# Kernel tuning notes

Hardware: AMD Instinct MI355X
Metric: run time of the kernel (lower is better)

The kernel has to match this reference:

```python
import jax, jax.numpy as jnp
import numpy as np


def _conv1x1(x, W, b):
    # x: [b,c,h,w], W: [out,in], b: [out]
    return jnp.einsum('oi,bihw->bohw', W, x) + b[None, :, None, None]


def setup_inputs() -> dict:
    key = jax.random.key(0)
    ks = jax.random.split(key, 8)
    B, C, H, W = 4, 256, 64, 64
    s = 1.0 / np.sqrt(C)
    return {
        'x1': jax.random.normal(ks[0], (B, C, H, W), jnp.float32),
        'x2': jax.random.normal(ks[1], (B, C, H, W), jnp.float32),
        'Wq': jax.random.normal(ks[2], (C, C), jnp.float32) * s,
        'bq': jax.random.normal(ks[3], (C,), jnp.float32) * 0.01,
        'Wk': jax.random.normal(ks[4], (C, C), jnp.float32) * s,
        'bk': jax.random.normal(ks[5], (C,), jnp.float32) * 0.01,
        'Wv': jax.random.normal(ks[6], (C, C), jnp.float32) * s,
        'bv': jax.random.normal(ks[7], (C,), jnp.float32) * 0.01,
    }


def reference(x1, x2, Wq, bq, Wk, bk, Wv, bv):
    b, c, h, w = x1.shape
    n = h * w
    q = _conv1x1(x1, Wq, bq).reshape(b, c, n)   # [b,c,n]
    k = _conv1x1(x2, Wk, bk).reshape(b, c, n)   # [b,c,n]
    v = _conv1x1(x2, Wv, bv).reshape(b, c, n)   # [b,c,n]
    # scores[b,i,j] = sum_c q[b,c,i] * k[b,c,j]; softmax over j (last dim)
    scores = jnp.einsum('bci,bcj->bij', q, k)
    attn = jax.nn.softmax(scores, axis=-1)      # [b,n,n]
    # out[b,c,i] = sum_j v[b,c,j] * attn[b,i,j]  (v @ attn^T)
    out = jnp.einsum('bcj,bij->bci', v, attn)
    return out.reshape(b, c, h, w)
```

## Files before the change

### kernel.cpp

```cpp
#include <hip/hip_runtime.h>

#define BATCH 4
#define CDIM 256
#define NDIM 4096
#define SPLITS 4
#define KSPLIT (NDIM / SPLITS)
#define JT 32
#define NTILES (KSPLIT / JT)

typedef unsigned short u16;
typedef unsigned int u32;
typedef _Float16 f16;
typedef __attribute__((ext_vector_type(8))) _Float16 half8;
typedef __attribute__((ext_vector_type(4))) float floatx4;

__device__ __forceinline__ void load_lds_128(const void* g, void* l) {
  __builtin_amdgcn_global_load_lds(
      (const __attribute__((address_space(1))) u32*)g,
      (__attribute__((address_space(3))) u32*)l, 16, 0, 0);
}

__global__ __launch_bounds__(256) void prep_w_k(
    const float* __restrict__ wq, const float* __restrict__ wk,
    const float* __restrict__ wv, f16* __restrict__ whq,
    f16* __restrict__ whk, f16* __restrict__ whv) {
  const int gid = blockIdx.x * 256 + threadIdx.x;
  const int a = gid >> 13;
  const int r = gid & 8191;
  const float* src = (a == 0) ? wq : ((a == 1) ? wk : wv);
  f16* dst = (a == 0) ? whq : ((a == 1) ? whk : whv);
  float4 v0 = *(const float4*)(src + r * 8);
  float4 v1 = *(const float4*)(src + r * 8 + 4);
  half8 h;
  h[0] = (f16)v0.x; h[1] = (f16)v0.y; h[2] = (f16)v0.z; h[3] = (f16)v0.w;
  h[4] = (f16)v1.x; h[5] = (f16)v1.y; h[6] = (f16)v1.z; h[7] = (f16)v1.w;
  *(half8*)(dst + r * 8) = h;
}

__global__ __launch_bounds__(256, 2) void proj_fused_k(
    const float* __restrict__ x1, const float* __restrict__ x2,
    const f16* __restrict__ whq, const float* __restrict__ bq,
    const f16* __restrict__ whk, const float* __restrict__ bk,
    const f16* __restrict__ whv, const float* __restrict__ bv,
    f16* __restrict__ qt, f16* __restrict__ kt, f16* __restrict__ vsp) {
  __shared__ __align__(16) u16 xt[256 * 132];
  const int j0 = blockIdx.x * 128;
  const int b = blockIdx.y;
  const int proj = blockIdx.z;
  const float* xs = ((proj == 0) ? x1 : x2) + (size_t)b * CDIM * NDIM;
  const int t = threadIdx.x;
#pragma unroll
  for (int it = 0; it < 32; ++it) {
    const int flat = t + it * 256;
    const int c = flat >> 5;
    const int n4 = (flat & 31) << 2;
    float4 v = *(const float4*)(xs + (size_t)c * NDIM + j0 + n4);
    union { f16 h[4]; uint2 u; } pk;
    pk.h[0] = (f16)v.x; pk.h[1] = (f16)v.y; pk.h[2] = (f16)v.z; pk.h[3] = (f16)v.w;
    *(uint2*)&xt[c * 132 + n4] = pk.u;
  }
  __syncthreads();
  const int wave = t >> 6, lane = t & 63, l16 = lane & 15, grp = lane >> 4;
  const f16* xth = (const f16*)xt;

  if (proj < 2) {
    const f16* w = proj ? whk : whq;
    const float* bias = proj ? bk : bq;
    f16* outp = (proj ? kt : qt) + (size_t)b * NDIM * CDIM;
    floatx4 acc[2][16];
#pragma unroll
    for (int mb = 0; mb < 2; ++mb)
#pragma unroll
      for (int nb = 0; nb < 16; ++nb) acc[mb][nb] = (floatx4){0.f, 0.f, 0.f, 0.f};
#pragma unroll
    for (int ks = 0; ks < 8; ++ks) {
      half8 a[2];
#pragma unroll
      for (int mb = 0; mb < 2; ++mb) {
        const int n = wave * 32 + mb * 16 + l16;
        half8 av;
#pragma unroll
        for (int jj = 0; jj < 8; ++jj)
          av[jj] = xth[(ks * 32 + grp * 8 + jj) * 132 + n];
        a[mb] = av;
      }
#pragma unroll
      for (int nb = 0; nb < 16; ++nb) {
        half8 bb = *(const half8*)(w + (size_t)(nb * 16 + l16) * CDIM + ks * 32 + grp * 8);
        acc[0][nb] = __builtin_amdgcn_mfma_f32_16x16x32_f16(a[0], bb, acc[0][nb], 0, 0, 0);
        acc[1][nb] = __builtin_amdgcn_mfma_f32_16x16x32_f16(a[1], bb, acc[1][nb], 0, 0, 0);
      }
    }
#pragma unroll
    for (int nb = 0; nb < 16; ++nb) {
      const int c = nb * 16 + l16;
      const float bvv = bias[c];
#pragma unroll
      for (int mb = 0; mb < 2; ++mb) {
        const int jbase = j0 + wave * 32 + mb * 16 + grp * 4;
#pragma unroll
        for (int r = 0; r < 4; ++r)
          outp[(size_t)(jbase + r) * CDIM + c] = (f16)(acc[mb][nb][r] + bvv);
      }
    }
  } else {
    f16* outp = vsp + (size_t)b * CDIM * NDIM;
    const int cw = (wave & 1) * 128;
    const int jw = (wave >> 1) * 64;
    floatx4 acc[8][4];
#pragma unroll
    for (int mb = 0; mb < 8; ++mb)
#pragma unroll
      for (int nb = 0; nb < 4; ++nb) acc[mb][nb] = (floatx4){0.f, 0.f, 0.f, 0.f};
#pragma unroll
    for (int ks = 0; ks < 8; ++ks) {
      half8 a[8];
#pragma unroll
      for (int mb = 0; mb < 8; ++mb)
        a[mb] = *(const half8*)(whv + (size_t)(cw + mb * 16 + l16) * CDIM + ks * 32 + grp * 8);
#pragma unroll
      for (int nb = 0; nb < 4; ++nb) {
        const int n = jw + nb * 16 + l16;
        half8 bv8;
#pragma unroll
        for (int jj = 0; jj < 8; ++jj)
          bv8[jj] = xth[(ks * 32 + grp * 8 + jj) * 132 + n];
#pragma unroll
        for (int mb = 0; mb < 8; ++mb)
          acc[mb][nb] = __builtin_amdgcn_mfma_f32_16x16x32_f16(a[mb], bv8, acc[mb][nb], 0, 0, 0);
      }
    }
#pragma unroll
    for (int mb = 0; mb < 8; ++mb)
#pragma unroll
      for (int r = 0; r < 4; ++r) {
        const int c = cw + mb * 16 + grp * 4 + r;
        const float bvv = bv[c];
#pragma unroll
        for (int nb = 0; nb < 4; ++nb) {
          const int j = j0 + jw + nb * 16 + l16;
          outp[(size_t)c * NDIM + j] = (f16)(acc[mb][nb][r] + bvv);
        }
      }
  }
}

__global__ __launch_bounds__(256, 2) void flash_k(
    const f16* __restrict__ qt, const f16* __restrict__ kt,
    const f16* __restrict__ vs, f16* __restrict__ pO,
    float* __restrict__ pm, float* __restrict__ pl) {
  __shared__ __align__(16) u16 smem[32768 + 2560];
  const int bx = blockIdx.x;
  const int c16 = bx & 15;
  const int b = c16 >> 2, s = c16 & 3;
  const int i0 = (bx >> 4) * 128;
  const int jwin = s * KSPLIT;
  const f16* Q = qt + (size_t)b * NDIM * CDIM;
  const f16* K = kt + (size_t)b * NDIM * CDIM;
  const f16* V = vs + (size_t)b * CDIM * NDIM;
  const int tid = threadIdx.x;
  const int wave = tid >> 6, lane = tid & 63, l16 = lane & 15, grp = lane >> 4;
  f16* Pw = (f16*)(smem + 32768) + wave * (16 * 40);

  half8 qf[2][8];
#pragma unroll
  for (int mb = 0; mb < 2; ++mb)
#pragma unroll
    for (int ks = 0; ks < 8; ++ks)
      qf[mb][ks] = *(const half8*)(Q + (size_t)(i0 + wave * 32 + mb * 16 + l16) * CDIM +
                                   ks * 32 + grp * 8);

  floatx4 O[2][16];
#pragma unroll
  for (int mb = 0; mb < 2; ++mb)
#pragma unroll
    for (int cb = 0; cb < 16; ++cb) O[mb][cb] = (floatx4){0.f, 0.f, 0.f, 0.f};
  float m_[2] = {-1e30f, -1e30f};
  float lsum[2] = {0.f, 0.f};

  const int kr2 = lane >> 5, kp = lane & 31;
  const int vrow = lane >> 2, vp = lane & 3;

#define STAGE(J0, BUF)                                                         \
  {                                                                            \
    u16* sK = smem + (BUF) * 16384;                                            \
    u16* sV = sK + 8192;                                                       \
    _Pragma("unroll") for (int it = 0; it < 4; ++it) {                         \
      const int row = wave * 8 + it * 2 + kr2;                                 \
      const int g = kp ^ (row & 7);                                            \
      load_lds_128(K + (size_t)((J0) + row) * CDIM + g * 8,                    \
                   &sK[(wave * 8 + it * 2) * 256]);                            \
    }                                                                          \
    _Pragma("unroll") for (int it = 0; it < 4; ++it) {                         \
      const int c = wave * 64 + it * 16 + vrow;                                \
      const int g = vp ^ ((c >> 2) & 3);                                       \
      load_lds_128(V + (size_t)c * NDIM + (J0) + g * 8,                        \
                   &sV[(wave * 64 + it * 16) * 32]);                           \
    }                                                                          \
  }

  STAGE(jwin, 0)

  for (int tt = 0; tt < NTILES; ++tt) {
    __syncthreads();
    if (tt + 1 < NTILES) STAGE(jwin + (tt + 1) * JT, (tt + 1) & 1)
    u16* bK = smem + (tt & 1) * 16384;
    u16* bV = bK + 8192;

    floatx4 S[2][2];
#pragma unroll
    for (int mb = 0; mb < 2; ++mb)
#pragma unroll
      for (int jb = 0; jb < 2; ++jb) S[mb][jb] = (floatx4){0.f, 0.f, 0.f, 0.f};
#pragma unroll
    for (int ks = 0; ks < 8; ++ks) {
      const int chunk = ks * 4 + grp;
#pragma unroll
      for (int jb = 0; jb < 2; ++jb) {
        const int row = jb * 16 + l16;
        half8 kf = *(const half8*)&bK[row * 256 + ((chunk ^ (row & 7)) << 3)];
        S[0][jb] = __builtin_amdgcn_mfma_f32_16x16x32_f16(qf[0][ks], kf, S[0][jb], 0, 0, 0);
        S[1][jb] = __builtin_amdgcn_mfma_f32_16x16x32_f16(qf[1][ks], kf, S[1][jb], 0, 0, 0);
      }
    }

    float alpha[2];
    half8 pa[2];
#pragma unroll
    for (int mb = 0; mb < 2; ++mb) {
#pragma unroll
      for (int jb = 0; jb < 2; ++jb)
#pragma unroll
        for (int r = 0; r < 4; ++r)
          Pw[(grp * 4 + r) * 40 + jb * 16 + l16] = (f16)S[mb][jb][r];
      half8 rawh = *(const half8*)&Pw[l16 * 40 + grp * 8];
      float u[8];
#pragma unroll
      for (int j = 0; j < 8; ++j) u[j] = (float)rawh[j];
      float mx = fmaxf(fmaxf(fmaxf(u[0], u[1]), fmaxf(u[2], u[3])),
                       fmaxf(fmaxf(u[4], u[5]), fmaxf(u[6], u[7])));
      mx = fmaxf(mx, __shfl_xor(mx, 16, 64));
      mx = fmaxf(mx, __shfl_xor(mx, 32, 64));
      const float mnew = fmaxf(m_[mb], mx);
      alpha[mb] = __expf(m_[mb] - mnew);
      m_[mb] = mnew;
      float pe[8];
#pragma unroll
      for (int j = 0; j < 8; ++j) pe[j] = __expf(u[j] - mnew);
      const float ps = ((pe[0] + pe[1]) + (pe[2] + pe[3])) +
                       ((pe[4] + pe[5]) + (pe[6] + pe[7]));
      lsum[mb] = lsum[mb] * alpha[mb] + ps;
      half8 h;
#pragma unroll
      for (int j = 0; j < 8; ++j) h[j] = (f16)pe[j];
      pa[mb] = h;
    }

    if (__any(alpha[0] < 1.f) || __any(alpha[1] < 1.f)) {
#pragma unroll
      for (int mb = 0; mb < 2; ++mb)
#pragma unroll
        for (int cb = 0; cb < 16; ++cb) O[mb][cb] *= alpha[mb];
    }

#pragma unroll
    for (int cb = 0; cb < 16; ++cb) {
      const int c = cb * 16 + l16;
      half8 vf = *(const half8*)&bV[c * 32 + ((grp ^ ((c >> 2) & 3)) << 3)];
      O[0][cb] = __builtin_amdgcn_mfma_f32_16x16x32_f16(vf, pa[0], O[0][cb], 0, 0, 0);
      O[1][cb] = __builtin_amdgcn_mfma_f32_16x16x32_f16(vf, pa[1], O[1][cb], 0, 0, 0);
    }
  }

#pragma unroll
  for (int mb = 0; mb < 2; ++mb) {
    lsum[mb] += __shfl_xor(lsum[mb], 16, 64);
    lsum[mb] += __shfl_xor(lsum[mb], 32, 64);
  }
  if (grp == 0) {
    const int base = (b * SPLITS + s) * NDIM + i0;
#pragma unroll
    for (int mb = 0; mb < 2; ++mb) {
      const int i = wave * 32 + mb * 16 + l16;
      pm[base + i] = m_[mb];
      pl[base + i] = lsum[mb];
    }
  }

  const size_t pbase = (size_t)(b * SPLITS + s) * CDIM * NDIM;
#pragma unroll
  for (int mb = 0; mb < 2; ++mb) {
    const int i = i0 + wave * 32 + mb * 16 + l16;
#pragma unroll
    for (int cb = 0; cb < 16; ++cb) {
      const int c = cb * 16 + grp * 4;
#pragma unroll
      for (int r = 0; r < 4; ++r)
        pO[pbase + (size_t)(c + r) * NDIM + i] = (f16)O[mb][cb][r];
    }
  }
}

__global__ __launch_bounds__(256) void combine_k(
    const f16* __restrict__ pO, const float* __restrict__ pm,
    const float* __restrict__ pl, float* __restrict__ out) {
  __shared__ float su[SPLITS][64];
  const int b = blockIdx.x >> 6;
  const int i0 = (blockIdx.x & 63) * 64;
  const int t = threadIdx.x;
  if (t < 64) {
    const int i = i0 + t;
    float mv[SPLITS], w[SPLITS];
    float M = -3e38f;
#pragma unroll
    for (int s = 0; s < SPLITS; ++s) {
      mv[s] = pm[(b * SPLITS + s) * NDIM + i];
      M = fmaxf(M, mv[s]);
    }
    float L = 0.f;
#pragma unroll
    for (int s = 0; s < SPLITS; ++s) {
      w[s] = __expf(mv[s] - M);
      L += pl[(b * SPLITS + s) * NDIM + i] * w[s];
    }
    const float invL = 1.0f / L;
#pragma unroll
    for (int s = 0; s < SPLITS; ++s) su[s][t] = w[s] * invL;
  }
  __syncthreads();
#pragma unroll
  for (int it = 0; it < 8; ++it) {
    const int task = t + it * 256;
    const int c = task >> 3, p = (task & 7) * 8;
    float acc[8] = {0.f, 0.f, 0.f, 0.f, 0.f, 0.f, 0.f, 0.f};
#pragma unroll
    for (int s = 0; s < SPLITS; ++s) {
      const f16* src = pO + ((size_t)(b * SPLITS + s) * CDIM + c) * NDIM + i0 + p;
      half8 h = *(const half8*)src;
#pragma unroll
      for (int j = 0; j < 8; ++j) acc[j] += su[s][p + j] * (float)h[j];
    }
    float* dst = out + ((size_t)b * CDIM + c) * NDIM + i0 + p;
    float4 lo = {acc[0], acc[1], acc[2], acc[3]};
    float4 hi = {acc[4], acc[5], acc[6], acc[7]};
    *(float4*)dst = lo;
    *(float4*)(dst + 4) = hi;
  }
}

extern "C" void kernel_launch(void* const* d_in, const int* in_sizes, int n_in,
                              void* d_out, int out_size, void* d_ws, size_t ws_size,
                              hipStream_t stream) {
  const float* x1 = (const float*)d_in[0];
  const float* x2 = (const float*)d_in[1];
  const float* Wq = (const float*)d_in[2];
  const float* bq = (const float*)d_in[3];
  const float* Wk = (const float*)d_in[4];
  const float* bk = (const float*)d_in[5];
  const float* Wv = (const float*)d_in[6];
  const float* bv = (const float*)d_in[7];
  float* out = (float*)d_out;
  char* ws = (char*)d_ws;
  f16* qtp = (f16*)(ws + 0);
  f16* ktp = (f16*)(ws + 8388608);
  f16* vsp = (f16*)(ws + 16777216);
  f16* whq = (f16*)(ws + 41943040);
  f16* whk = whq + CDIM * CDIM;
  f16* whv = whk + CDIM * CDIM;
  f16* pO = (f16*)(ws + 25165824);
  float* pm = (float*)(ws + 58720256);
  float* pl = (float*)(ws + 58982400);

  prep_w_k<<<dim3(96), dim3(256), 0, stream>>>(Wq, Wk, Wv, whq, whk, whv);
  proj_fused_k<<<dim3(NDIM / 128, BATCH, 3), dim3(256), 0, stream>>>(
      x1, x2, whq, bq, whk, bk, whv, bv, qtp, ktp, vsp);
  flash_k<<<dim3(512), dim3(256), 0, stream>>>(qtp, ktp, vsp, pO, pm, pl);
  combine_k<<<dim3(256), dim3(256), 0, stream>>>(pO, pm, pl, out);
}
```

Before: 255.7 us.

## Swap QK MFMA operands, redistribute P via shuffles, lazily rescale softmax

The score MFMA operands are swapped so each lane holds score values along j. The probabilities are then converted to the PV-MFMA operand layout with cross-lane shuffles instead of a per-wave LDS round trip, which removes the extra LDS buffer and its store/load latency. The running max is only updated and the accumulators rescaled when the new tile max exceeds the old one by more than 8, skipping most rescale work. The risk is extra shuffle instructions, reloading V fragments per mb, and exp values up to e^8 that must stay within fp16 range.

New measurement: 375.4 us. 46.8% more time.

```diff
diff --git a/kernel.cpp b/kernel.cpp
--- a/kernel.cpp
+++ b/kernel.cpp
@@ -149,7 +149,7 @@
     const f16* __restrict__ qt, const f16* __restrict__ kt,
     const f16* __restrict__ vs, f16* __restrict__ pO,
     float* __restrict__ pm, float* __restrict__ pl) {
-  __shared__ __align__(16) u16 smem[32768 + 2560];
+  __shared__ __align__(16) u16 smem[32768];
   const int bx = blockIdx.x;
   const int c16 = bx & 15;
   const int b = c16 >> 2, s = c16 & 3;
@@ -160,7 +160,9 @@
   const f16* V = vs + (size_t)b * CDIM * NDIM;
   const int tid = threadIdx.x;
   const int wave = tid >> 6, lane = tid & 63, l16 = lane & 15, grp = lane >> 4;
-  f16* Pw = (f16*)(smem + 32768) + wave * (16 * 40);
+  const int shA = ((grp & 1) << 5) + l16;
+  const int shB = shA + 16;
+  const bool hi = (grp & 2) != 0;
 
   half8 qf[2][8];
 #pragma unroll
@@ -219,56 +221,56 @@
       for (int jb = 0; jb < 2; ++jb) {
         const int row = jb * 16 + l16;
         half8 kf = *(const half8*)&bK[row * 256 + ((chunk ^ (row & 7)) << 3)];
-        S[0][jb] = __builtin_amdgcn_mfma_f32_16x16x32_f16(qf[0][ks], kf, S[0][jb], 0, 0, 0);
-        S[1][jb] = __builtin_amdgcn_mfma_f32_16x16x32_f16(qf[1][ks], kf, S[1][jb], 0, 0, 0);
-      }
-    }
-
-    float alpha[2];
-    half8 pa[2];
+        S[0][jb] = __builtin_amdgcn_mfma_f32_16x16x32_f16(kf, qf[0][ks], S[0][jb], 0, 0, 0);
+        S[1][jb] = __builtin_amdgcn_mfma_f32_16x16x32_f16(kf, qf[1][ks], S[1][jb], 0, 0, 0);
+      }
+    }
+
 #pragma unroll
     for (int mb = 0; mb < 2; ++mb) {
+      float u[8];
 #pragma unroll
       for (int jb = 0; jb < 2; ++jb)
 #pragma unroll
-        for (int r = 0; r < 4; ++r)
-          Pw[(grp * 4 + r) * 40 + jb * 16 + l16] = (f16)S[mb][jb][r];
-      half8 rawh = *(const half8*)&Pw[l16 * 40 + grp * 8];
-      float u[8];
-#pragma unroll
-      for (int j = 0; j < 8; ++j) u[j] = (float)rawh[j];
+        for (int r = 0; r < 4; ++r) u[jb * 4 + r] = S[mb][jb][r];
       float mx = fmaxf(fmaxf(fmaxf(u[0], u[1]), fmaxf(u[2], u[3])),
                        fmaxf(fmaxf(u[4], u[5]), fmaxf(u[6], u[7])));
       mx = fmaxf(mx, __shfl_xor(mx, 16, 64));
       mx = fmaxf(mx, __shfl_xor(mx, 32, 64));
-      const float mnew = fmaxf(m_[mb], mx);
-      alpha[mb] = __expf(m_[mb] - mnew);
-      m_[mb] = mnew;
+      if (!__all(mx - m_[mb] <= 8.0f)) {
+        const float mnew = fmaxf(m_[mb], mx);
+        const float al = __expf(m_[mb] - mnew);
+        m_[mb] = mnew;
+        lsum[mb] *= al;
+#pragma unroll
+        for (int cb = 0; cb < 16; ++cb) O[mb][cb] *= al;
+      }
+      const float mm = m_[mb];
       float pe[8];
 #pragma unroll
-      for (int j = 0; j < 8; ++j) pe[j] = __expf(u[j] - mnew);
-      const float ps = ((pe[0] + pe[1]) + (pe[2] + pe[3])) +
-                       ((pe[4] + pe[5]) + (pe[6] + pe[7]));
-      lsum[mb] = lsum[mb] * alpha[mb] + ps;
-      half8 h;
-#pragma unroll
-      for (int j = 0; j < 8; ++j) h[j] = (f16)pe[j];
-      pa[mb] = h;
-    }
-
-    if (__any(alpha[0] < 1.f) || __any(alpha[1] < 1.f)) {
-#pragma unroll
-      for (int mb = 0; mb < 2; ++mb)
-#pragma unroll
-        for (int cb = 0; cb < 16; ++cb) O[mb][cb] *= alpha[mb];
-    }
-
-#pragma unroll
-    for (int cb = 0; cb < 16; ++cb) {
-      const int c = cb * 16 + l16;
-      half8 vf = *(const half8*)&bV[c * 32 + ((grp ^ ((c >> 2) & 3)) << 3)];
-      O[0][cb] = __builtin_amdgcn_mfma_f32_16x16x32_f16(vf, pa[0], O[0][cb], 0, 0, 0);
-      O[1][cb] = __builtin_amdgcn_mfma_f32_16x16x32_f16(vf, pa[1], O[1][cb], 0, 0, 0);
+      for (int j = 0; j < 8; ++j) pe[j] = __expf(u[j] - mm);
+      lsum[mb] += ((pe[0] + pe[1]) + (pe[2] + pe[3])) +
+                  ((pe[4] + pe[5]) + (pe[6] + pe[7]));
+      union HW { half8 h; u32 w[4]; };
+      HW pk;
+#pragma unroll
+      for (int j = 0; j < 8; ++j) pk.h[j] = (f16)pe[j];
+      const u32 a0 = __shfl(pk.w[0], shA), a1 = __shfl(pk.w[1], shA);
+      const u32 a2 = __shfl(pk.w[2], shA), a3 = __shfl(pk.w[3], shA);
+      const u32 b0 = __shfl(pk.w[0], shB), b1 = __shfl(pk.w[1], shB);
+      const u32 b2 = __shfl(pk.w[2], shB), b3 = __shfl(pk.w[3], shB);
+      HW pa;
+      pa.w[0] = hi ? a2 : a0;
+      pa.w[1] = hi ? a3 : a1;
+      pa.w[2] = hi ? b2 : b0;
+      pa.w[3] = hi ? b3 : b1;
+
+#pragma unroll
+      for (int cb = 0; cb < 16; ++cb) {
+        const int c = cb * 16 + l16;
+        half8 vf = *(const half8*)&bV[c * 32 + ((grp ^ ((c >> 2) & 3)) << 3)];
+        O[mb][cb] = __builtin_amdgcn_mfma_f32_16x16x32_f16(vf, pa.h, O[mb][cb], 0, 0, 0);
+      }
     }
   }
 
```

## Halve flash query tile per block and read V directly from global memory

Applied to the files above, without the earlier changes.

Each flash block now handles 64 query rows instead of 128, with one 16-row MFMA tile per wave. The grid doubles and launch bounds allow 4 blocks per CU. V is no longer staged through LDS; each wave reads its V fragments straight from global memory, which halves the LDS footprint and register pressure. The trade-off is less K/V reuse per block: K is streamed twice as often, and the uncoalesced global V reads per MFMA sit in the inner loop and may stall it.

Measured after the change: 442.0 us. 1.73x slower.

```diff
diff --git a/kernel.cpp b/kernel.cpp
--- a/kernel.cpp
+++ b/kernel.cpp
@@ -145,58 +145,45 @@
   }
 }
 
-__global__ __launch_bounds__(256, 2) void flash_k(
+__global__ __launch_bounds__(256, 4) void flash_k(
     const f16* __restrict__ qt, const f16* __restrict__ kt,
     const f16* __restrict__ vs, f16* __restrict__ pO,
     float* __restrict__ pm, float* __restrict__ pl) {
-  __shared__ __align__(16) u16 smem[32768 + 2560];
+  __shared__ __align__(16) u16 smem[16384 + 2560];
   const int bx = blockIdx.x;
   const int c16 = bx & 15;
   const int b = c16 >> 2, s = c16 & 3;
-  const int i0 = (bx >> 4) * 128;
+  const int i0 = (bx >> 4) * 64;
   const int jwin = s * KSPLIT;
   const f16* Q = qt + (size_t)b * NDIM * CDIM;
   const f16* K = kt + (size_t)b * NDIM * CDIM;
-  const f16* V = vs + (size_t)b * CDIM * NDIM;
+  const f16* V = vs + (size_t)b * CDIM * NDIM + jwin;
   const int tid = threadIdx.x;
   const int wave = tid >> 6, lane = tid & 63, l16 = lane & 15, grp = lane >> 4;
-  f16* Pw = (f16*)(smem + 32768) + wave * (16 * 40);
-
-  half8 qf[2][8];
-#pragma unroll
-  for (int mb = 0; mb < 2; ++mb)
-#pragma unroll
-    for (int ks = 0; ks < 8; ++ks)
-      qf[mb][ks] = *(const half8*)(Q + (size_t)(i0 + wave * 32 + mb * 16 + l16) * CDIM +
-                                   ks * 32 + grp * 8);
-
-  floatx4 O[2][16];
-#pragma unroll
-  for (int mb = 0; mb < 2; ++mb)
-#pragma unroll
-    for (int cb = 0; cb < 16; ++cb) O[mb][cb] = (floatx4){0.f, 0.f, 0.f, 0.f};
-  float m_[2] = {-1e30f, -1e30f};
-  float lsum[2] = {0.f, 0.f};
+  f16* Pw = (f16*)(smem + 16384) + wave * (16 * 40);
+
+  half8 qf[8];
+#pragma unroll
+  for (int ks = 0; ks < 8; ++ks)
+    qf[ks] = *(const half8*)(Q + (size_t)(i0 + wave * 16 + l16) * CDIM + ks * 32 + grp * 8);
+
+  floatx4 O[16];
+#pragma unroll
+  for (int cb = 0; cb < 16; ++cb) O[cb] = (floatx4){0.f, 0.f, 0.f, 0.f};
+  float m_ = -1e30f;
+  float lsum = 0.f;
 
   const int kr2 = lane >> 5, kp = lane & 31;
-  const int vrow = lane >> 2, vp = lane & 3;
 
 #define STAGE(J0, BUF)                                                         \
   {                                                                            \
-    u16* sK = smem + (BUF) * 16384;                                            \
-    u16* sV = sK + 8192;                                                       \
+    u16* sK = smem + (BUF) * 8192;                                             \
     _Pragma("unroll") for (int it = 0; it < 4; ++it) {                         \
       const int row = wave * 8 + it * 2 + kr2;                                 \
       const int g = kp ^ (row & 7);                                            \
       load_lds_128(K + (size_t)((J0) + row) * CDIM + g * 8,                    \
                    &sK[(wave * 8 + it * 2) * 256]);                            \
     }                                                                          \
-    _Pragma("unroll") for (int it = 0; it < 4; ++it) {                         \
-      const int c = wave * 64 + it * 16 + vrow;                                \
-      const int g = vp ^ ((c >> 2) & 3);                                       \
-      load_lds_128(V + (size_t)c * NDIM + (J0) + g * 8,                        \
-                   &sV[(wave * 64 + it * 16) * 32]);                           \
-    }                                                                          \
   }
 
   STAGE(jwin, 0)
@@ -204,14 +191,12 @@
   for (int tt = 0; tt < NTILES; ++tt) {
     __syncthreads();
     if (tt + 1 < NTILES) STAGE(jwin + (tt + 1) * JT, (tt + 1) & 1)
-    u16* bK = smem + (tt & 1) * 16384;
-    u16* bV = bK + 8192;
-
-    floatx4 S[2][2];
-#pragma unroll
-    for (int mb = 0; mb < 2; ++mb)
-#pragma unroll
-      for (int jb = 0; jb < 2; ++jb) S[mb][jb] = (floatx4){0.f, 0.f, 0.f, 0.f};
+    u16* bK = smem + (tt & 1) * 8192;
+    const f16* Vt = V + tt * JT;
+
+    floatx4 S[2];
+#pragma unroll
+    for (int jb = 0; jb < 2; ++jb) S[jb] = (floatx4){0.f, 0.f, 0.f, 0.f};
 #pragma unroll
     for (int ks = 0; ks < 8; ++ks) {
       const int chunk = ks * 4 + grp;
@@ -219,85 +204,66 @@
       for (int jb = 0; jb < 2; ++jb) {
         const int row = jb * 16 + l16;
         half8 kf = *(const half8*)&bK[row * 256 + ((chunk ^ (row & 7)) << 3)];
-        S[0][jb] = __builtin_amdgcn_mfma_f32_16x16x32_f16(qf[0][ks], kf, S[0][jb], 0, 0, 0);
-        S[1][jb] = __builtin_amdgcn_mfma_f32_16x16x32_f16(qf[1][ks], kf, S[1][jb], 0, 0, 0);
-      }
-    }
-
-    float alpha[2];
-    half8 pa[2];
-#pragma unroll
-    for (int mb = 0; mb < 2; ++mb) {
-#pragma unroll
-      for (int jb = 0; jb < 2; ++jb)
-#pragma unroll
-        for (int r = 0; r < 4; ++r)
-          Pw[(grp * 4 + r) * 40 + jb * 16 + l16] = (f16)S[mb][jb][r];
-      half8 rawh = *(const half8*)&Pw[l16 * 40 + grp * 8];
-      float u[8];
-#pragma unroll
-      for (int j = 0; j < 8; ++j) u[j] = (float)rawh[j];
-      float mx = fmaxf(fmaxf(fmaxf(u[0], u[1]), fmaxf(u[2], u[3])),
-                       fmaxf(fmaxf(u[4], u[5]), fmaxf(u[6], u[7])));
-      mx = fmaxf(mx, __shfl_xor(mx, 16, 64));
-      mx = fmaxf(mx, __shfl_xor(mx, 32, 64));
-      const float mnew = fmaxf(m_[mb], mx);
-      alpha[mb] = __expf(m_[mb] - mnew);
-      m_[mb] = mnew;
-      float pe[8];
-#pragma unroll
-      for (int j = 0; j < 8; ++j) pe[j] = __expf(u[j] - mnew);
-      const float ps = ((pe[0] + pe[1]) + (pe[2] + pe[3])) +
-                       ((pe[4] + pe[5]) + (pe[6] + pe[7]));
-      lsum[mb] = lsum[mb] * alpha[mb] + ps;
-      half8 h;
-#pragma unroll
-      for (int j = 0; j < 8; ++j) h[j] = (f16)pe[j];
-      pa[mb] = h;
-    }
-
-    if (__any(alpha[0] < 1.f) || __any(alpha[1] < 1.f)) {
-#pragma unroll
-      for (int mb = 0; mb < 2; ++mb)
-#pragma unroll
-        for (int cb = 0; cb < 16; ++cb) O[mb][cb] *= alpha[mb];
+        S[jb] = __builtin_amdgcn_mfma_f32_16x16x32_f16(qf[ks], kf, S[jb], 0, 0, 0);
+      }
+    }
+
+#pragma unroll
+    for (int jb = 0; jb < 2; ++jb)
+#pragma unroll
+      for (int r = 0; r < 4; ++r)
+        Pw[(grp * 4 + r) * 40 + jb * 16 + l16] = (f16)S[jb][r];
+    half8 rawh = *(const half8*)&Pw[l16 * 40 + grp * 8];
+    float u[8];
+#pragma unroll
+    for (int j = 0; j < 8; ++j) u[j] = (float)rawh[j];
+    float mx = fmaxf(fmaxf(fmaxf(u[0], u[1]), fmaxf(u[2], u[3])),
+                     fmaxf(fmaxf(u[4], u[5]), fmaxf(u[6], u[7])));
+    mx = fmaxf(mx, __shfl_xor(mx, 16, 64));
+    mx = fmaxf(mx, __shfl_xor(mx, 32, 64));
+    const float mnew = fmaxf(m_, mx);
+    const float alpha = __expf(m_ - mnew);
+    m_ = mnew;
+    float pe[8];
+#pragma unroll
+    for (int j = 0; j < 8; ++j) pe[j] = __expf(u[j] - mnew);
+    const float ps = ((pe[0] + pe[1]) + (pe[2] + pe[3])) +
+                     ((pe[4] + pe[5]) + (pe[6] + pe[7]));
+    lsum = lsum * alpha + ps;
+    half8 pa;
+#pragma unroll
+    for (int j = 0; j < 8; ++j) pa[j] = (f16)pe[j];
+
+    if (__any(alpha < 1.f)) {
+#pragma unroll
+      for (int cb = 0; cb < 16; ++cb) O[cb] *= alpha;
     }
 
 #pragma unroll
     for (int cb = 0; cb < 16; ++cb) {
       const int c = cb * 16 + l16;
-      half8 vf = *(const half8*)&bV[c * 32 + ((grp ^ ((c >> 2) & 3)) << 3)];
-      O[0][cb] = __builtin_amdgcn_mfma_f32_16x16x32_f16(vf, pa[0], O[0][cb], 0, 0, 0);
-      O[1][cb] = __builtin_amdgcn_mfma_f32_16x16x32_f16(vf, pa[1], O[1][cb], 0, 0, 0);
-    }
-  }
-
-#pragma unroll
-  for (int mb = 0; mb < 2; ++mb) {
-    lsum[mb] += __shfl_xor(lsum[mb], 16, 64);
-    lsum[mb] += __shfl_xor(lsum[mb], 32, 64);
-  }
+      half8 vf = *(const half8*)(Vt + (size_t)c * NDIM + grp * 8);
+      O[cb] = __builtin_amdgcn_mfma_f32_16x16x32_f16(vf, pa, O[cb], 0, 0, 0);
+    }
+  }
+
+  lsum += __shfl_xor(lsum, 16, 64);
+  lsum += __shfl_xor(lsum, 32, 64);
   if (grp == 0) {
     const int base = (b * SPLITS + s) * NDIM + i0;
-#pragma unroll
-    for (int mb = 0; mb < 2; ++mb) {
-      const int i = wave * 32 + mb * 16 + l16;
-      pm[base + i] = m_[mb];
-      pl[base + i] = lsum[mb];
-    }
+    const int i = wave * 16 + l16;
+    pm[base + i] = m_;
+    pl[base + i] = lsum;
   }
 
   const size_t pbase = (size_t)(b * SPLITS + s) * CDIM * NDIM;
-#pragma unroll
-  for (int mb = 0; mb < 2; ++mb) {
-    const int i = i0 + wave * 32 + mb * 16 + l16;
-#pragma unroll
-    for (int cb = 0; cb < 16; ++cb) {
-      const int c = cb * 16 + grp * 4;
-#pragma unroll
-      for (int r = 0; r < 4; ++r)
-        pO[pbase + (size_t)(c + r) * NDIM + i] = (f16)O[mb][cb][r];
-    }
+  const int i = i0 + wave * 16 + l16;
+#pragma unroll
+  for (int cb = 0; cb < 16; ++cb) {
+    const int c = cb * 16 + grp * 4;
+#pragma unroll
+    for (int r = 0; r < 4; ++r)
+      pO[pbase + (size_t)(c + r) * NDIM + i] = (f16)O[cb][r];
   }
 }
 
@@ -374,6 +340,6 @@
   prep_w_k<<<dim3(96), dim3(256), 0, stream>>>(Wq, Wk, Wv, whq, whk, whv);
   proj_fused_k<<<dim3(NDIM / 128, BATCH, 3), dim3(256), 0, stream>>>(
       x1, x2, whq, bq, whk, bk, whv, bv, qtp, ktp, vsp);
-  flash_k<<<dim3(512), dim3(256), 0, stream>>>(qtp, ktp, vsp, pO, pm, pl);
+  flash_k<<<dim3(1024), dim3(256), 0, stream>>>(qtp, ktp, vsp, pO, pm, pl);
   combine_k<<<dim3(256), dim3(256), 0, stream>>>(pO, pm, pl, out);
 }
```
